# Performance work log

Hardware: AMD Instinct MI355X
Metric: run time of the kernel (lower is better)

The kernel has to match this reference:

```python
import jax, jax.numpy as jnp
import numpy as np

B, T, D, H = 512, 64, 16, 1024  # H must equal T*D (required by the original reshape)


def setup_inputs() -> dict:
    key = jax.random.key(0)
    ks = list(jax.random.split(key, 30))
    def nrm(k, shape, s=0.05):
        return jax.random.normal(k, shape, dtype=jnp.float32) * s
    inp = {}
    inp["values"] = jax.random.normal(ks[0], (B, T, D), dtype=jnp.float32)
    inp["masks"] = (jax.random.uniform(ks[1], (B, T, D)) < 0.8).astype(jnp.float32)
    i = 2
    for pre in ("fw", "bw"):
        for l, din in ((0, D), (1, H)):
            inp[f"{pre}_Wih{l}"] = nrm(ks[i], (4 * H, din)); i += 1
            inp[f"{pre}_Whh{l}"] = nrm(ks[i], (4 * H, H)); i += 1
            inp[f"{pre}_bih{l}"] = nrm(ks[i], (4 * H,)); i += 1
            inp[f"{pre}_bhh{l}"] = nrm(ks[i], (4 * H,)); i += 1
    inp["out_W"] = nrm(ks[i], (D, H)); i += 1
    inp["out_b"] = nrm(ks[i], (D,)); i += 1
    inp["fcb_W"] = nrm(ks[i], (D, 1)); i += 1
    inp["fcb_b"] = nrm(ks[i], (D,)); i += 1
    inp["fce_W"] = nrm(ks[i], (D, 1)); i += 1
    inp["fce_b"] = nrm(ks[i], (D,)); i += 1
    return inp


def _lstm_cell(x, h, c, Wih, Whh, bih, bhh):
    # PyTorch LSTMCell: gate order i, f, g, o
    gates = x @ Wih.T + bih + h @ Whh.T + bhh
    i, f, g, o = jnp.split(gates, 4, axis=-1)
    c2 = jax.nn.sigmoid(f) * c + jax.nn.sigmoid(i) * jnp.tanh(g)
    return jax.nn.sigmoid(o) * jnp.tanh(c2), c2


def _forward(values, masks, fw_Wih0, fw_Whh0, fw_bih0, fw_bhh0, fw_Wih1, fw_Whh1, fw_bih1, fw_bhh1,
             bw_Wih0, bw_Whh0, bw_bih0, bw_bhh0, bw_Wih1, bw_Whh1, bw_bih1, bw_bhh1,
             out_W, out_b, fcb_W, fcb_b, fce_W, fce_b):
    Bc, Tc, Dc = values.shape
    zeros = jnp.zeros((Bc, H), values.dtype)
    bwd_values = jnp.flip(values, 1)
    bwd_masks = jnp.flip(masks, 1)
    # fc_begin/fc_end outputs are dead code in the original (init loop starts at layer 1)
    # Original pre-loop: layers 1..L-1 run once with zero inputs/states.
    hf1, cf1 = _lstm_cell(zeros, zeros, zeros, fw_Wih1, fw_Whh1, fw_bih1, fw_bhh1)
    hb1, cb1 = _lstm_cell(zeros, zeros, zeros, bw_Wih1, bw_Whh1, bw_bih1, bw_bhh1)
    carry0 = (zeros, zeros, hf1, cf1, zeros, zeros, hb1, cb1)

    def step(carry, xs):
        hf0, cf0, hf1, cf1, hb0, cb0, hb1, cb1 = carry
        x_f, m_f, x_b, m_b = xs
        cc_f = (1.0 - m_f) * (hf1 @ out_W.T + out_b) + m_f * x_f
        cc_b = (1.0 - m_b) * (hb1 @ out_W.T + out_b) + m_b * x_b
        hf0, cf0 = _lstm_cell(cc_f, hf0, cf0, fw_Wih0, fw_Whh0, fw_bih0, fw_bhh0)
        hf1, cf1 = _lstm_cell(hf0, hf1, cf1, fw_Wih1, fw_Whh1, fw_bih1, fw_bhh1)
        hb0, cb0 = _lstm_cell(cc_b, hb0, cb0, bw_Wih0, bw_Whh0, bw_bih0, bw_bhh0)
        hb1, cb1 = _lstm_cell(hb0, hb1, cb1, bw_Wih1, bw_Whh1, bw_bih1, bw_bhh1)
        return (hf0, cf0, hf1, cf1, hb0, cb0, hb1, cb1), None

    xs = (jnp.swapaxes(values, 0, 1), jnp.swapaxes(masks, 0, 1),
          jnp.swapaxes(bwd_values, 0, 1), jnp.swapaxes(bwd_masks, 0, 1))
    carry, _ = jax.lax.scan(step, carry0, xs)
    hf1, hb1 = carry[2], carry[6]
    # Original averages fwd with hidden-dim-flipped bwd hidden state
    h = (hf1 + jnp.flip(hb1, 1)) * 0.5
    imputations = h.reshape(Bc, Tc, Dc)
    imputed = imputations * (1.0 - masks) + values * masks
    return h, imputations, imputed


def reference(values, masks, fw_Wih0, fw_Whh0, fw_bih0, fw_bhh0, fw_Wih1, fw_Whh1, fw_bih1, fw_bhh1,
              bw_Wih0, bw_Whh0, bw_bih0, bw_bhh0, bw_Wih1, bw_Whh1, bw_bih1, bw_bhh1,
              out_W, out_b, fcb_W, fcb_b, fce_W, fce_b):
    return _forward(values, masks, fw_Wih0, fw_Whh0, fw_bih0, fw_bhh0, fw_Wih1, fw_Whh1, fw_bih1, fw_bhh1,
                    bw_Wih0, bw_Whh0, bw_bih0, bw_bhh0, bw_Wih1, bw_Whh1, bw_bih1, bw_bhh1,
                    out_W, out_b, fcb_W, fcb_b, fce_W, fce_b)
```

## Files before the change

kernel.cpp:

```cpp
#include <hip/hip_runtime.h>
#include <cstdint>
#include <cstddef>

typedef unsigned short u16;
typedef __attribute__((ext_vector_type(8))) short short8;
typedef __attribute__((ext_vector_type(4))) short short4v;
typedef __attribute__((ext_vector_type(4))) float f32x4;

#define NB 512
#define NT 64
#define ND 16
#define NH 1024

__device__ __forceinline__ u16 f2bf(float x) {
  union { float f; unsigned u; } v; v.f = x;
  unsigned r = v.u + 0x7fffu + ((v.u >> 16) & 1u);
  return (u16)(r >> 16);
}
__device__ __forceinline__ float bf2f(u16 u) {
  union { float f; unsigned u; } v; v.u = ((unsigned)u) << 16;
  return v.f;
}
__device__ __forceinline__ float sigf(float x) { return 1.f / (1.f + __expf(-x)); }

__device__ __forceinline__ int swz(int row, int col) {
  return ((((col >> 3) ^ (row & 7)) << 3) | (col & 7));
}

__device__ __forceinline__ int inv_np(int np) {
  int hb = np >> 6, g = (np >> 4) & 3, hlo = np & 15;
  return g * 1024 + hb * 16 + hlo;
}

__global__ void k_prep_big(const float* s0, const float* s1, const float* s2,
                           const float* s3, const float* s4, const float* s5, u16* dst) {
  for (unsigned q = blockIdx.x * 256 + threadIdx.x; q < (6u << 20); q += gridDim.x * 256) {
    int mat = q >> 20;
    int rem = q & ((1 << 20) - 1);
    int np = rem >> 8;
    int k = (rem & 255) * 4;
    int row = inv_np(np);
    const float* s = mat == 0 ? s0 : mat == 1 ? s1 : mat == 2 ? s2 : mat == 3 ? s3 : mat == 4 ? s4 : s5;
    float4 v = *(const float4*)(s + (size_t)row * NH + k);
    int nb = np >> 4, fr = np & 15, kb = k >> 5, fq = (k >> 3) & 3, e = k & 7;
    u16* d = dst + (size_t)mat * 4194304 + (size_t)((nb * 32 + kb) * 64 + fq * 16 + fr) * 8 + e;
    d[0] = f2bf(v.x); d[1] = f2bf(v.y); d[2] = f2bf(v.z); d[3] = f2bf(v.w);
  }
}

__global__ void k_prep_small(const float* fwih0, const float* bwih0,
                             const float* fbi0, const float* fbh0, const float* fbi1, const float* fbh1,
                             const float* bbi0, const float* bbh0, const float* bbi1, const float* bbh1,
                             const float* outW,
                             u16* wih0p, float* biasb, u16* owbf) {
  int idx = blockIdx.x * 256 + threadIdx.x;
  if (idx < 524288) {
    int dir = idx >> 18;
    int r = idx & 262143;
    int np = r >> 6, d = r & 63;
    int row = inv_np(np);
    const float* s = dir ? bwih0 : fwih0;
    float v = (d < 16) ? s[row * 16 + d] : 0.f;
    int nb = np >> 4, fr = np & 15, kb = d >> 5, fq = (d >> 3) & 3, e = d & 7;
    wih0p[(size_t)dir * 262144 + (size_t)((nb * 2 + kb) * 64 + fq * 16 + fr) * 8 + e] = f2bf(v);
  } else if (idx < 524288 + 16384) {
    int j = idx - 524288;
    int which = j >> 12;
    int np = j & 4095;
    int row = inv_np(np);
    const float* bi = which == 0 ? fbi0 : which == 1 ? fbi1 : which == 2 ? bbi0 : bbi1;
    const float* bh = which == 0 ? fbh0 : which == 1 ? fbh1 : which == 2 ? bbh0 : bbh1;
    biasb[which * 4096 + np] = bi[row] + bh[row];
  } else if (idx < 524288 + 16384 + 16384) {
    int j = idx - 524288 - 16384;
    owbf[j] = f2bf(outW[j]);
  }
}

__global__ void k_init(const float* fbi1, const float* fbh1, const float* bbi1, const float* bbh1,
                       float* c0, float* c1, u16* h0bf, u16* h1bf) {
  int idx = blockIdx.x * 256 + threadIdx.x;
  int dir = idx >> 19;
  int rem = idx & ((1 << 19) - 1);
  int b = rem >> 10, h = rem & 1023;
  const float* bi = dir ? bbi1 : fbi1;
  const float* bh = dir ? bbh1 : fbh1;
  float gi = bi[h] + bh[h];
  float gg = bi[2048 + h] + bh[2048 + h];
  float go = bi[3072 + h] + bh[3072 + h];
  float c = sigf(gi) * tanhf(gg);
  float hv = sigf(go) * tanhf(c);
  size_t o = (size_t)dir * 524288 + rem;
  c1[o] = c;
  h1bf[(size_t)(dir * 2) * 524288 + (size_t)b * NH + swz(b, h)] = f2bf(hv);
  c0[o] = 0.f;
  h0bf[(size_t)(dir * 2) * 524288 + rem] = 0;
}

__global__ __launch_bounds__(256) void k_cc0(const u16* h1f, const u16* h1b,
                                             const float* outW, float* partial) {
  int dir = blockIdx.y;
  int w = threadIdx.x >> 6, lane = threadIdx.x & 63;
  int b = blockIdx.x * 4 + w;
  const u16* hb = dir ? h1b : h1f;
  int key = b & 7;
  short8 ha = *(const short8*)(hb + (size_t)b * NH + ((lane * 2) ^ key) * 8);
  short8 hc = *(const short8*)(hb + (size_t)b * NH + ((lane * 2 + 1) ^ key) * 8);
  float hf[16];
#pragma unroll
  for (int j = 0; j < 8; ++j) { hf[j] = bf2f((u16)ha[j]); hf[8 + j] = bf2f((u16)hc[j]); }
  float sums[16];
#pragma unroll
  for (int d = 0; d < 16; ++d) {
    const float* wr = outW + (size_t)d * NH + lane * 16;
    float s = 0.f;
#pragma unroll
    for (int j = 0; j < 16; ++j) s += hf[j] * wr[j];
#pragma unroll
    for (int off = 32; off; off >>= 1) s += __shfl_xor(s, off);
    sums[d] = s;
  }
  if (lane == 0) {
    float* dst = partial + (size_t)dir * 524288 + (size_t)b * 16;
#pragma unroll
    for (int d = 0; d < 16; ++d) dst[d] = sums[d];
  }
}

struct Frags { short8 a[4]; short8 b[8]; };

__device__ __forceinline__ void domfma(const Frags& F, f32x4 (&acc)[2][4]) {
#pragma unroll
  for (int kk = 0; kk < 2; ++kk)
#pragma unroll
    for (int mi = 0; mi < 2; ++mi)
#pragma unroll
      for (int ni = 0; ni < 4; ++ni)
        acc[mi][ni] = __builtin_amdgcn_mfma_f32_16x16x32_bf16(F.a[mi * 2 + kk], F.b[ni * 2 + kk],
                                                              acc[mi][ni], 0, 0, 0);
}

struct StepCtx {
  u16* h0bf; u16* h1bf;
  const u16* wbig; const u16* wih0p;
  const float* biasb;
  float* c0; float* c1;
  float* partial;
  const float* values; const float* masks; const float* outb;
  const u16* owbf;
};

__device__ __forceinline__ void phase_g0(u16* SM, const StepCtx& a, int dir,
                                         int m_blk, int n_blk, int t, int p) {
  const int m0 = m_blk * 64, n0 = n_blk * 128;
  const int tid = threadIdx.x, w = tid >> 6, lane = tid & 63;
  const int wm = w >> 1, wn = w & 1;
  const int fr = lane & 15, fq = lane >> 4, key = fr & 7;
  const int lane8 = lane * 8;
  const int nbb = n_blk * 8 + wn * 4;
  const u16* h0_in = a.h0bf + (size_t)(dir * 2 + p) * 524288;
  u16* h0_out = a.h0bf + (size_t)(dir * 2 + 1 - p) * 524288;
  const u16* W00 = a.wbig + (size_t)(dir * 3 + 0) * 4194304;
  const u16* Wcc = a.wih0p + (size_t)dir * 262144;
  const float* bias0 = a.biasb + (size_t)dir * 2 * 4096;
  float* cs0 = a.c0 + (size_t)dir * 524288;
  const u16* hA = h0_in + (size_t)m0 * NH;

  int voffA[4];
#pragma unroll
  for (int mi = 0; mi < 2; ++mi)
#pragma unroll
    for (int kk = 0; kk < 2; ++kk)
      voffA[mi * 2 + kk] = (wm * 32 + mi * 16 + fr) * NH + ((fq + kk * 4) ^ key) * 8;

  f32x4 acc[2][4];
#pragma unroll
  for (int i = 0; i < 2; ++i)
#pragma unroll
    for (int j = 0; j < 4; ++j) acc[i][j] = f32x4{0.f, 0.f, 0.f, 0.f};

  Frags f0, fA, fB;
#pragma unroll
  for (int ni = 0; ni < 4; ++ni)
#pragma unroll
    for (int kk = 0; kk < 2; ++kk)
      f0.b[ni * 2 + kk] = *(const short8*)(Wcc + (size_t)((nbb + ni) * 2 + kk) * 512 + lane8);
  auto LD0 = [&](int c, Frags& F) {
    int ci = c - 1;
#pragma unroll
    for (int i = 0; i < 4; ++i) F.a[i] = *(const short8*)(hA + ci * 64 + voffA[i]);
#pragma unroll
    for (int ni = 0; ni < 4; ++ni)
#pragma unroll
      for (int kk = 0; kk < 2; ++kk)
        F.b[ni * 2 + kk] = *(const short8*)(W00 + (size_t)((nbb + ni) * 32 + ci * 2 + kk) * 512 + lane8);
  };
  LD0(1, fA); LD0(2, fB);

  {
    const int rl = tid >> 2, q = tid & 3;
    const int grow = m0 + rl;
    const int d4 = q * 4;
    float4 ps = {0.f, 0.f, 0.f, 0.f};
    const float* pp = a.partial + (size_t)dir * 524288 + (size_t)grow * 16 + d4;
    for (int nb = 0; nb < 64; ++nb) {
      float4 v = *(const float4*)(pp + (size_t)nb * 8192);
      ps.x += v.x; ps.y += v.y; ps.z += v.z; ps.w += v.w;
    }
    int tt = dir ? (NT - 1 - t) : t;
    float4 x = *(const float4*)(a.values + ((size_t)grow * NT + tt) * ND + d4);
    float4 m = *(const float4*)(a.masks + ((size_t)grow * NT + tt) * ND + d4);
    float4 ob = *(const float4*)(a.outb + d4);
    short4v cc;
    cc[0] = (short)f2bf((1.f - m.x) * (ps.x + ob.x) + m.x * x.x);
    cc[1] = (short)f2bf((1.f - m.y) * (ps.y + ob.y) + m.y * x.y);
    cc[2] = (short)f2bf((1.f - m.z) * (ps.z + ob.z) + m.z * x.z);
    cc[3] = (short)f2bf((1.f - m.w) * (ps.w + ob.w) + m.w * x.w);
    int k2 = rl & 7;
    *(short4v*)(SM + rl * 64 + (((d4 >> 3) ^ k2) << 3) + (d4 & 7)) = cc;
    short8 z8 = {0, 0, 0, 0, 0, 0, 0, 0};
    *(short8*)(SM + rl * 64 + (((2 + q) ^ k2) << 3)) = z8;
    if (q < 2) *(short8*)(SM + rl * 64 + (((6 + q) ^ k2) << 3)) = z8;
    asm volatile("s_waitcnt lgkmcnt(0)" ::: "memory");
    __builtin_amdgcn_sched_barrier(0);
  }
  __builtin_amdgcn_s_barrier();

#pragma unroll
  for (int mi = 0; mi < 2; ++mi)
#pragma unroll
    for (int kk = 0; kk < 2; ++kk)
      f0.a[mi * 2 + kk] = *(const short8*)(SM + (wm * 32 + mi * 16 + fr) * 64 + ((fq + kk * 4) ^ key) * 8);
  domfma(f0, acc);
  for (int c = 1; c < 17; c += 2) {
    domfma(fA, acc);
    if (c + 2 < 17) LD0(c + 2, fA);
    domfma(fB, acc);
    if (c + 3 < 17) LD0(c + 3, fB);
  }

  const int hg = ((n0 + wn * 64) >> 2) + fr;
  const float b0 = bias0[n0 + wn * 64 + fr];
  const float b1 = bias0[n0 + wn * 64 + 16 + fr];
  const float b2 = bias0[n0 + wn * 64 + 32 + fr];
  const float b3 = bias0[n0 + wn * 64 + 48 + fr];
#pragma unroll
  for (int mi = 0; mi < 2; ++mi)
#pragma unroll
    for (int r = 0; r < 4; ++r) {
      int row = m0 + wm * 32 + mi * 16 + fq * 4 + r;
      size_t sidx = (size_t)row * NH + hg;
      float iv = acc[mi][0][r] + b0;
      float fv = acc[mi][1][r] + b1;
      float gv = acc[mi][2][r] + b2;
      float ov = acc[mi][3][r] + b3;
      float cp = cs0[sidx];
      float c2 = sigf(fv) * cp + sigf(iv) * tanhf(gv);
      float hvv = sigf(ov) * tanhf(c2);
      cs0[sidx] = c2;
      h0_out[(size_t)row * NH + swz(row, hg)] = f2bf(hvv);
    }
}

__device__ __forceinline__ void phase_g1(u16* SM, const StepCtx& a, int dir,
                                         int m_blk, int n_blk, int t, int p) {
  const int m0 = m_blk * 64, n0 = n_blk * 128;
  const int tid = threadIdx.x, w = tid >> 6, lane = tid & 63;
  const int wm = w >> 1, wn = w & 1;
  const int fr = lane & 15, fq = lane >> 4, key = fr & 7;
  const int lane8 = lane * 8;
  const int nbb = n_blk * 8 + wn * 4;
  const u16* h0_new = a.h0bf + (size_t)(dir * 2 + 1 - p) * 524288;
  const u16* h1_in = a.h1bf + (size_t)(dir * 2 + p) * 524288;
  u16* h1_out = a.h1bf + (size_t)(dir * 2 + 1 - p) * 524288;
  const u16* W10 = a.wbig + (size_t)(dir * 3 + 1) * 4194304;
  const u16* W11 = a.wbig + (size_t)(dir * 3 + 2) * 4194304;
  const float* bias1 = a.biasb + (size_t)(dir * 2 + 1) * 4096;
  float* cs1 = a.c1 + (size_t)dir * 524288;
  const u16* hA0 = h0_new + (size_t)m0 * NH;
  const u16* hA1 = h1_in + (size_t)m0 * NH;

  int voffA[4];
#pragma unroll
  for (int mi = 0; mi < 2; ++mi)
#pragma unroll
    for (int kk = 0; kk < 2; ++kk)
      voffA[mi * 2 + kk] = (wm * 32 + mi * 16 + fr) * NH + ((fq + kk * 4) ^ key) * 8;

  f32x4 acc[2][4];
#pragma unroll
  for (int i = 0; i < 2; ++i)
#pragma unroll
    for (int j = 0; j < 4; ++j) acc[i][j] = f32x4{0.f, 0.f, 0.f, 0.f};

  auto LD1 = [&](int c, Frags& F) {
    const u16* ha = (c < 16) ? hA0 : hA1;
    const u16* wb = (c < 16) ? W10 : W11;
    int ci = (c < 16) ? c : c - 16;
#pragma unroll
    for (int i = 0; i < 4; ++i) F.a[i] = *(const short8*)(ha + ci * 64 + voffA[i]);
#pragma unroll
    for (int ni = 0; ni < 4; ++ni)
#pragma unroll
      for (int kk = 0; kk < 2; ++kk)
        F.b[ni * 2 + kk] = *(const short8*)(wb + (size_t)((nbb + ni) * 32 + ci * 2 + kk) * 512 + lane8);
  };

  Frags fA, fB;
  LD1(0, fA); LD1(1, fB);
  for (int c = 0; c < 32; c += 2) {
    domfma(fA, acc);
    if (c + 2 < 32) LD1(c + 2, fA);
    domfma(fB, acc);
    if (c + 3 < 32) LD1(c + 3, fB);
  }

  const int hb4 = (n0 + wn * 64) >> 2;
  const int hg = hb4 + fr;
  const float b0 = bias1[n0 + wn * 64 + fr];
  const float b1 = bias1[n0 + wn * 64 + 16 + fr];
  const float b2 = bias1[n0 + wn * 64 + 32 + fr];
  const float b3 = bias1[n0 + wn * 64 + 48 + fr];
  float hsv[2][4];
#pragma unroll
  for (int mi = 0; mi < 2; ++mi)
#pragma unroll
    for (int r = 0; r < 4; ++r) {
      int row = m0 + wm * 32 + mi * 16 + fq * 4 + r;
      size_t sidx = (size_t)row * NH + hg;
      float iv = acc[mi][0][r] + b0;
      float fv = acc[mi][1][r] + b1;
      float gv = acc[mi][2][r] + b2;
      float ov = acc[mi][3][r] + b3;
      float cp = cs1[sidx];
      float c2 = sigf(fv) * cp + sigf(iv) * tanhf(gv);
      float hvv = sigf(ov) * tanhf(c2);
      cs1[sidx] = c2;
      h1_out[(size_t)row * NH + swz(row, hg)] = f2bf(hvv);
      hsv[mi][r] = hvv;
    }

  {
    u16* ts = SM + w * 512;
    *(short4v*)(ts + (lane >> 2) * 32 + 16 + (lane & 3) * 4) = short4v{0, 0, 0, 0};
    short8 afr = {0, 0, 0, 0, 0, 0, 0, 0};
    if (fq < 2) afr = *(const short8*)(a.owbf + (size_t)fr * NH + hb4 + fq * 8);
    float* pout = a.partial + ((size_t)(dir * 64 + n_blk * 2 + wn) * 512) * 16;
#pragma unroll
    for (int mi = 0; mi < 2; ++mi) {
#pragma unroll
      for (int r = 0; r < 4; ++r)
        *(ts + (fq * 4 + r) * 32 + fr) = f2bf(hsv[mi][r]);
      asm volatile("s_waitcnt lgkmcnt(0)" ::: "memory");
      __builtin_amdgcn_sched_barrier(0);
      short8 bfr2 = *(const short8*)(ts + fr * 32 + fq * 8);
      f32x4 pz = {0.f, 0.f, 0.f, 0.f};
      pz = __builtin_amdgcn_mfma_f32_16x16x32_bf16(afr, bfr2, pz, 0, 0, 0);
      int row = m0 + wm * 32 + mi * 16 + fr;
      float4 st = {pz[0], pz[1], pz[2], pz[3]};
      *(float4*)(pout + (size_t)row * 16 + fq * 4) = st;
      asm volatile("s_waitcnt lgkmcnt(0)" ::: "memory");
      __builtin_amdgcn_sched_barrier(0);
    }
  }
}

__global__ __launch_bounds__(256) void k_g0(StepCtx a, int t) {
  __shared__ u16 SM[4096];
  phase_g0(SM, a, blockIdx.z, blockIdx.y, blockIdx.x, t, t & 1);
}
__global__ __launch_bounds__(256) void k_g1(StepCtx a, int t) {
  __shared__ u16 SM[4096];
  phase_g1(SM, a, blockIdx.z, blockIdx.y, blockIdx.x, t, t & 1);
}

__global__ void k_final(const u16* hf1, const u16* hb1, const float* values,
                        const float* masks, float* out) {
  int idx = blockIdx.x * 256 + threadIdx.x;
  int b = idx >> 10, j = idx & 1023;
  float hf = bf2f(hf1[(size_t)b * NH + swz(b, j)]);
  int jr = NH - 1 - j;
  float hb = bf2f(hb1[(size_t)b * NH + swz(b, jr)]);
  float hv = 0.5f * (hf + hb);
  float m = masks[idx];
  out[idx] = hv;
  out[524288 + idx] = hv;
  out[1048576 + idx] = hv * (1.f - m) + values[idx] * m;
}

extern "C" void kernel_launch(void* const* d_in, const int* in_sizes, int n_in,
                              void* d_out, int out_size, void* d_ws, size_t ws_size,
                              hipStream_t stream) {
  const float* values  = (const float*)d_in[0];
  const float* masks   = (const float*)d_in[1];
  const float* fw_Wih0 = (const float*)d_in[2];
  const float* fw_Whh0 = (const float*)d_in[3];
  const float* fw_bih0 = (const float*)d_in[4];
  const float* fw_bhh0 = (const float*)d_in[5];
  const float* fw_Wih1 = (const float*)d_in[6];
  const float* fw_Whh1 = (const float*)d_in[7];
  const float* fw_bih1 = (const float*)d_in[8];
  const float* fw_bhh1 = (const float*)d_in[9];
  const float* bw_Wih0 = (const float*)d_in[10];
  const float* bw_Whh0 = (const float*)d_in[11];
  const float* bw_bih0 = (const float*)d_in[12];
  const float* bw_bhh0 = (const float*)d_in[13];
  const float* bw_Wih1 = (const float*)d_in[14];
  const float* bw_Whh1 = (const float*)d_in[15];
  const float* bw_bih1 = (const float*)d_in[16];
  const float* bw_bhh1 = (const float*)d_in[17];
  const float* out_W   = (const float*)d_in[18];
  const float* out_b   = (const float*)d_in[19];

  char* ws = (char*)d_ws;
  u16* wbig    = (u16*)ws;
  u16* wih0p   = (u16*)(ws + 50331648);
  float* biasb = (float*)(ws + 51380224);
  u16* owbf    = (u16*)(ws + 51445760);
  float* c0    = (float*)(ws + 51478528);
  float* c1    = (float*)(ws + 55672832);
  u16* h0bf    = (u16*)(ws + 59867136);
  u16* h1bf    = (u16*)(ws + 64061440);
  float* partial = (float*)(ws + 68255744);
  if (ws_size < 72450048) return;

  k_prep_big<<<4096, 256, 0, stream>>>(fw_Whh0, fw_Wih1, fw_Whh1, bw_Whh0, bw_Wih1, bw_Whh1, wbig);
  k_prep_small<<<2176, 256, 0, stream>>>(fw_Wih0, bw_Wih0, fw_bih0, fw_bhh0, fw_bih1, fw_bhh1,
                                         bw_bih0, bw_bhh0, bw_bih1, bw_bhh1, out_W,
                                         wih0p, biasb, owbf);
  k_init<<<4096, 256, 0, stream>>>(fw_bih1, fw_bhh1, bw_bih1, bw_bhh1, c0, c1, h0bf, h1bf);
  hipMemsetAsync(partial, 0, 4194304, stream);
  k_cc0<<<dim3(128, 2), 256, 0, stream>>>(h1bf, h1bf + (size_t)2 * 524288, out_W, partial);

  StepCtx sc;
  sc.h0bf = h0bf; sc.h1bf = h1bf;
  sc.wbig = wbig; sc.wih0p = wih0p;
  sc.biasb = biasb; sc.c0 = c0; sc.c1 = c1;
  sc.partial = partial;
  sc.values = values; sc.masks = masks; sc.outb = out_b;
  sc.owbf = owbf;

  for (int t = 0; t < NT; ++t) {
    k_g0<<<dim3(32, 8, 2), 256, 0, stream>>>(sc, t);
    k_g1<<<dim3(32, 8, 2), 256, 0, stream>>>(sc, t);
  }

  k_final<<<2048, 256, 0, stream>>>(h1bf, h1bf + (size_t)2 * 524288, values, masks, (float*)d_out);
}
```

Measured before the change: 3.781 ms.

## Stage hidden-state A tiles through LDS with async global_load_lds multi-buffering

The recurrent GEMM kernels now copy the activation (A) tiles into a 4-deep LDS ring using global_load_lds, wait on them with explicit vmcnt counters and block barriers, and keep a triple-buffered register pipeline for the weight (B) fragments. This replaces direct global loads of A fragments per wave, which duplicated reads across waves, with shared staging and deeper prefetch, at the cost of more LDS per block and more barriers. Launch bounds now request two blocks per CU. The weight-prep kernel is also rewritten so each thread writes one coalesced 16-byte packed chunk, and the partial-sum reduction uses two accumulators.

```diff
diff --git a/kernel.cpp b/kernel.cpp
--- a/kernel.cpp
+++ b/kernel.cpp
@@ -12,6 +12,8 @@
 #define ND 16
 #define NH 1024
 
+#define WAITV(N) asm volatile("s_waitcnt vmcnt(" #N ")" ::: "memory")
+
 __device__ __forceinline__ u16 f2bf(float x) {
   union { float f; unsigned u; } v; v.f = x;
   unsigned r = v.u + 0x7fffu + ((v.u >> 16) & 1u);
@@ -23,6 +25,11 @@
 }
 __device__ __forceinline__ float sigf(float x) { return 1.f / (1.f + __expf(-x)); }
 
+__device__ __forceinline__ void glds16(const void* g, void* l) {
+  __builtin_amdgcn_global_load_lds((const __attribute__((address_space(1))) void*)g,
+                                   (__attribute__((address_space(3))) void*)l, 16, 0, 0);
+}
+
 __device__ __forceinline__ int swz(int row, int col) {
   return ((((col >> 3) ^ (row & 7)) << 3) | (col & 7));
 }
@@ -34,18 +41,22 @@
 
 __global__ void k_prep_big(const float* s0, const float* s1, const float* s2,
                            const float* s3, const float* s4, const float* s5, u16* dst) {
-  for (unsigned q = blockIdx.x * 256 + threadIdx.x; q < (6u << 20); q += gridDim.x * 256) {
-    int mat = q >> 20;
-    int rem = q & ((1 << 20) - 1);
-    int np = rem >> 8;
-    int k = (rem & 255) * 4;
-    int row = inv_np(np);
-    const float* s = mat == 0 ? s0 : mat == 1 ? s1 : mat == 2 ? s2 : mat == 3 ? s3 : mat == 4 ? s4 : s5;
-    float4 v = *(const float4*)(s + (size_t)row * NH + k);
-    int nb = np >> 4, fr = np & 15, kb = k >> 5, fq = (k >> 3) & 3, e = k & 7;
-    u16* d = dst + (size_t)mat * 4194304 + (size_t)((nb * 32 + kb) * 64 + fq * 16 + fr) * 8 + e;
-    d[0] = f2bf(v.x); d[1] = f2bf(v.y); d[2] = f2bf(v.z); d[3] = f2bf(v.w);
-  }
+  unsigned q = blockIdx.x * 256 + threadIdx.x;
+  int mat = q >> 19;
+  int r = q & ((1 << 19) - 1);
+  int nb = r >> 11, kb = (r >> 6) & 31, l = r & 63;
+  int fr = l & 15, fq = l >> 4;
+  int np = nb * 16 + fr;
+  int row = inv_np(np);
+  int k0 = kb * 32 + fq * 8;
+  const float* s = mat == 0 ? s0 : mat == 1 ? s1 : mat == 2 ? s2 : mat == 3 ? s3 : mat == 4 ? s4 : s5;
+  const float* sr = s + (size_t)row * NH + k0;
+  float4 v0 = *(const float4*)sr;
+  float4 v1 = *(const float4*)(sr + 4);
+  short8 o;
+  o[0] = (short)f2bf(v0.x); o[1] = (short)f2bf(v0.y); o[2] = (short)f2bf(v0.z); o[3] = (short)f2bf(v0.w);
+  o[4] = (short)f2bf(v1.x); o[5] = (short)f2bf(v1.y); o[6] = (short)f2bf(v1.z); o[7] = (short)f2bf(v1.w);
+  *(short8*)(dst + (size_t)q * 8) = o;
 }
 
 __global__ void k_prep_small(const float* fwih0, const float* bwih0,
@@ -127,18 +138,7 @@
   }
 }
 
-struct Frags { short8 a[4]; short8 b[8]; };
-
-__device__ __forceinline__ void domfma(const Frags& F, f32x4 (&acc)[2][4]) {
-#pragma unroll
-  for (int kk = 0; kk < 2; ++kk)
-#pragma unroll
-    for (int mi = 0; mi < 2; ++mi)
-#pragma unroll
-      for (int ni = 0; ni < 4; ++ni)
-        acc[mi][ni] = __builtin_amdgcn_mfma_f32_16x16x32_bf16(F.a[mi * 2 + kk], F.b[ni * 2 + kk],
-                                                              acc[mi][ni], 0, 0, 0);
-}
+struct BF { short8 b[8]; };
 
 struct StepCtx {
   u16* h0bf; u16* h1bf;
@@ -150,10 +150,13 @@
   const u16* owbf;
 };
 
-__device__ __forceinline__ void phase_g0(u16* SM, const StepCtx& a, int dir,
-                                         int m_blk, int n_blk, int t, int p) {
+__global__ __launch_bounds__(256, 2) void k_g0(StepCtx a, int t) {
+  __shared__ u16 SM[5 * 4096];
+  const int dir = blockIdx.z, m_blk = blockIdx.y, n_blk = blockIdx.x;
+  const int p = t & 1;
   const int m0 = m_blk * 64, n0 = n_blk * 128;
   const int tid = threadIdx.x, w = tid >> 6, lane = tid & 63;
+  const int srow = lane >> 3, scol = (lane & 7) * 8;
   const int wm = w >> 1, wn = w & 1;
   const int fr = lane & 15, fq = lane >> 4, key = fr & 7;
   const int lane8 = lane * 8;
@@ -164,14 +167,13 @@
   const u16* Wcc = a.wih0p + (size_t)dir * 262144;
   const float* bias0 = a.biasb + (size_t)dir * 2 * 4096;
   float* cs0 = a.c0 + (size_t)dir * 524288;
-  const u16* hA = h0_in + (size_t)m0 * NH;
-
-  int voffA[4];
+
+  int aoff[4];
 #pragma unroll
   for (int mi = 0; mi < 2; ++mi)
 #pragma unroll
     for (int kk = 0; kk < 2; ++kk)
-      voffA[mi * 2 + kk] = (wm * 32 + mi * 16 + fr) * NH + ((fq + kk * 4) ^ key) * 8;
+      aoff[mi * 2 + kk] = (wm * 32 + mi * 16 + fr) * 64 + ((fq + kk * 4) ^ key) * 8;
 
   f32x4 acc[2][4];
 #pragma unroll
@@ -179,34 +181,66 @@
 #pragma unroll
     for (int j = 0; j < 4; ++j) acc[i][j] = f32x4{0.f, 0.f, 0.f, 0.f};
 
-  Frags f0, fA, fB;
-#pragma unroll
-  for (int ni = 0; ni < 4; ++ni)
-#pragma unroll
-    for (int kk = 0; kk < 2; ++kk)
-      f0.b[ni * 2 + kk] = *(const short8*)(Wcc + (size_t)((nbb + ni) * 2 + kk) * 512 + lane8);
-  auto LD0 = [&](int c, Frags& F) {
+  auto stageA = [&](int c) {
+    u16* lb = SM + (c & 3) * 4096;
+    const u16* pa = h0_in + (size_t)(c - 1) * 64;
+    glds16(pa + (size_t)(m0 + w * 16 + srow) * NH + scol, lb + (w * 16) * 64);
+    glds16(pa + (size_t)(m0 + w * 16 + 8 + srow) * NH + scol, lb + (w * 16 + 8) * 64);
+  };
+  auto LDB = [&](int c, BF& F) {
     int ci = c - 1;
-#pragma unroll
-    for (int i = 0; i < 4; ++i) F.a[i] = *(const short8*)(hA + ci * 64 + voffA[i]);
 #pragma unroll
     for (int ni = 0; ni < 4; ++ni)
 #pragma unroll
       for (int kk = 0; kk < 2; ++kk)
         F.b[ni * 2 + kk] = *(const short8*)(W00 + (size_t)((nbb + ni) * 32 + ci * 2 + kk) * 512 + lane8);
   };
-  LD0(1, fA); LD0(2, fB);
+  auto domfma = [&](const short8 (&af)[4], const BF& B) {
+#pragma unroll
+    for (int kk = 0; kk < 2; ++kk)
+#pragma unroll
+      for (int mi = 0; mi < 2; ++mi)
+#pragma unroll
+        for (int ni = 0; ni < 4; ++ni)
+          acc[mi][ni] = __builtin_amdgcn_mfma_f32_16x16x32_bf16(af[mi * 2 + kk], B.b[ni * 2 + kk],
+                                                                acc[mi][ni], 0, 0, 0);
+  };
+  auto DO = [&](int x, BF& B, int st, int lb) {
+    __builtin_amdgcn_s_barrier();
+    __builtin_amdgcn_sched_barrier(0);
+    if (st >= 0) stageA(st);
+    short8 af[4];
+    const u16* base = SM + (x & 3) * 4096;
+#pragma unroll
+    for (int i = 0; i < 4; ++i) af[i] = *(const short8*)(base + aoff[i]);
+    domfma(af, B);
+    if (lb >= 0) LDB(lb, B);
+  };
+
+  BF Ba, Bb, Bc;
+#pragma unroll
+  for (int ni = 0; ni < 4; ++ni)
+#pragma unroll
+    for (int kk = 0; kk < 2; ++kk)
+      Ba.b[ni * 2 + kk] = *(const short8*)(Wcc + (size_t)((nbb + ni) * 2 + kk) * 512 + lane8);
+  stageA(1); stageA(2); stageA(3);
+  LDB(1, Bb); LDB(2, Bc);
 
   {
+    u16* SM4 = SM + 4 * 4096;
     const int rl = tid >> 2, q = tid & 3;
     const int grow = m0 + rl;
     const int d4 = q * 4;
-    float4 ps = {0.f, 0.f, 0.f, 0.f};
+    float4 ps0 = {0.f, 0.f, 0.f, 0.f}, ps1 = {0.f, 0.f, 0.f, 0.f};
     const float* pp = a.partial + (size_t)dir * 524288 + (size_t)grow * 16 + d4;
-    for (int nb = 0; nb < 64; ++nb) {
-      float4 v = *(const float4*)(pp + (size_t)nb * 8192);
-      ps.x += v.x; ps.y += v.y; ps.z += v.z; ps.w += v.w;
+#pragma unroll 4
+    for (int nb = 0; nb < 64; nb += 2) {
+      float4 v0 = *(const float4*)(pp + (size_t)nb * 8192);
+      float4 v1 = *(const float4*)(pp + (size_t)(nb + 1) * 8192);
+      ps0.x += v0.x; ps0.y += v0.y; ps0.z += v0.z; ps0.w += v0.w;
+      ps1.x += v1.x; ps1.y += v1.y; ps1.z += v1.z; ps1.w += v1.w;
     }
+    float4 ps = {ps0.x + ps1.x, ps0.y + ps1.y, ps0.z + ps1.z, ps0.w + ps1.w};
     int tt = dir ? (NT - 1 - t) : t;
     float4 x = *(const float4*)(a.values + ((size_t)grow * NT + tt) * ND + d4);
     float4 m = *(const float4*)(a.masks + ((size_t)grow * NT + tt) * ND + d4);
@@ -217,27 +251,33 @@
     cc[2] = (short)f2bf((1.f - m.z) * (ps.z + ob.z) + m.z * x.z);
     cc[3] = (short)f2bf((1.f - m.w) * (ps.w + ob.w) + m.w * x.w);
     int k2 = rl & 7;
-    *(short4v*)(SM + rl * 64 + (((d4 >> 3) ^ k2) << 3) + (d4 & 7)) = cc;
+    *(short4v*)(SM4 + rl * 64 + (((d4 >> 3) ^ k2) << 3) + (d4 & 7)) = cc;
     short8 z8 = {0, 0, 0, 0, 0, 0, 0, 0};
-    *(short8*)(SM + rl * 64 + (((2 + q) ^ k2) << 3)) = z8;
-    if (q < 2) *(short8*)(SM + rl * 64 + (((6 + q) ^ k2) << 3)) = z8;
+    *(short8*)(SM4 + rl * 64 + (((2 + q) ^ k2) << 3)) = z8;
+    if (q < 2) *(short8*)(SM4 + rl * 64 + (((6 + q) ^ k2) << 3)) = z8;
     asm volatile("s_waitcnt lgkmcnt(0)" ::: "memory");
     __builtin_amdgcn_sched_barrier(0);
   }
+
   __builtin_amdgcn_s_barrier();
-
-#pragma unroll
-  for (int mi = 0; mi < 2; ++mi)
-#pragma unroll
-    for (int kk = 0; kk < 2; ++kk)
-      f0.a[mi * 2 + kk] = *(const short8*)(SM + (wm * 32 + mi * 16 + fr) * 64 + ((fq + kk * 4) ^ key) * 8);
-  domfma(f0, acc);
-  for (int c = 1; c < 17; c += 2) {
-    domfma(fA, acc);
-    if (c + 2 < 17) LD0(c + 2, fA);
-    domfma(fB, acc);
-    if (c + 3 < 17) LD0(c + 3, fB);
-  }
+  __builtin_amdgcn_sched_barrier(0);
+  {
+    short8 af[4];
+    const u16* SM4 = SM + 4 * 4096;
+#pragma unroll
+    for (int i = 0; i < 4; ++i) af[i] = *(const short8*)(SM4 + aoff[i]);
+    domfma(af, Ba);
+    LDB(3, Ba);
+  }
+  for (int c = 1; c < 13; c += 3) {
+    WAITV(28); DO(c, Bb, c + 3, c + 3);
+    WAITV(28); DO(c + 1, Bc, c + 4, c + 4);
+    WAITV(28); DO(c + 2, Ba, c + 5, c + 5);
+  }
+  WAITV(28); DO(13, Bb, 16, 16);
+  WAITV(28); DO(14, Bc, -1, -1);
+  WAITV(18); DO(15, Ba, -1, -1);
+  WAITV(8);  DO(16, Bb, -1, -1);
 
   const int hg = ((n0 + wn * 64) >> 2) + fr;
   const float b0 = bias0[n0 + wn * 64 + fr];
@@ -262,10 +302,13 @@
     }
 }
 
-__device__ __forceinline__ void phase_g1(u16* SM, const StepCtx& a, int dir,
-                                         int m_blk, int n_blk, int t, int p) {
+__global__ __launch_bounds__(256, 2) void k_g1(StepCtx a, int t) {
+  __shared__ u16 SM[4 * 4096];
+  const int dir = blockIdx.z, m_blk = blockIdx.y, n_blk = blockIdx.x;
+  const int p = t & 1;
   const int m0 = m_blk * 64, n0 = n_blk * 128;
   const int tid = threadIdx.x, w = tid >> 6, lane = tid & 63;
+  const int srow = lane >> 3, scol = (lane & 7) * 8;
   const int wm = w >> 1, wn = w & 1;
   const int fr = lane & 15, fq = lane >> 4, key = fr & 7;
   const int lane8 = lane * 8;
@@ -277,15 +320,13 @@
   const u16* W11 = a.wbig + (size_t)(dir * 3 + 2) * 4194304;
   const float* bias1 = a.biasb + (size_t)(dir * 2 + 1) * 4096;
   float* cs1 = a.c1 + (size_t)dir * 524288;
-  const u16* hA0 = h0_new + (size_t)m0 * NH;
-  const u16* hA1 = h1_in + (size_t)m0 * NH;
-
-  int voffA[4];
+
+  int aoff[4];
 #pragma unroll
   for (int mi = 0; mi < 2; ++mi)
 #pragma unroll
     for (int kk = 0; kk < 2; ++kk)
-      voffA[mi * 2 + kk] = (wm * 32 + mi * 16 + fr) * NH + ((fq + kk * 4) ^ key) * 8;
+      aoff[mi * 2 + kk] = (wm * 32 + mi * 16 + fr) * 64 + ((fq + kk * 4) ^ key) * 8;
 
   f32x4 acc[2][4];
 #pragma unroll
@@ -293,27 +334,57 @@
 #pragma unroll
     for (int j = 0; j < 4; ++j) acc[i][j] = f32x4{0.f, 0.f, 0.f, 0.f};
 
-  auto LD1 = [&](int c, Frags& F) {
-    const u16* ha = (c < 16) ? hA0 : hA1;
+  auto stageA = [&](int c) {
+    u16* lb = SM + (c & 3) * 4096;
+    const u16* pa = (c < 16) ? (h0_new + (size_t)c * 64) : (h1_in + (size_t)(c - 16) * 64);
+    glds16(pa + (size_t)(m0 + w * 16 + srow) * NH + scol, lb + (w * 16) * 64);
+    glds16(pa + (size_t)(m0 + w * 16 + 8 + srow) * NH + scol, lb + (w * 16 + 8) * 64);
+  };
+  auto LDB = [&](int c, BF& F) {
     const u16* wb = (c < 16) ? W10 : W11;
     int ci = (c < 16) ? c : c - 16;
 #pragma unroll
-    for (int i = 0; i < 4; ++i) F.a[i] = *(const short8*)(ha + ci * 64 + voffA[i]);
-#pragma unroll
     for (int ni = 0; ni < 4; ++ni)
 #pragma unroll
       for (int kk = 0; kk < 2; ++kk)
         F.b[ni * 2 + kk] = *(const short8*)(wb + (size_t)((nbb + ni) * 32 + ci * 2 + kk) * 512 + lane8);
   };
-
-  Frags fA, fB;
-  LD1(0, fA); LD1(1, fB);
-  for (int c = 0; c < 32; c += 2) {
-    domfma(fA, acc);
-    if (c + 2 < 32) LD1(c + 2, fA);
-    domfma(fB, acc);
-    if (c + 3 < 32) LD1(c + 3, fB);
-  }
+  auto domfma = [&](const short8 (&af)[4], const BF& B) {
+#pragma unroll
+    for (int kk = 0; kk < 2; ++kk)
+#pragma unroll
+      for (int mi = 0; mi < 2; ++mi)
+#pragma unroll
+        for (int ni = 0; ni < 4; ++ni)
+          acc[mi][ni] = __builtin_amdgcn_mfma_f32_16x16x32_bf16(af[mi * 2 + kk], B.b[ni * 2 + kk],
+                                                                acc[mi][ni], 0, 0, 0);
+  };
+  auto DO = [&](int x, BF& B, int st, int lb) {
+    __builtin_amdgcn_s_barrier();
+    __builtin_amdgcn_sched_barrier(0);
+    if (st >= 0) stageA(st);
+    short8 af[4];
+    const u16* base = SM + (x & 3) * 4096;
+#pragma unroll
+    for (int i = 0; i < 4; ++i) af[i] = *(const short8*)(base + aoff[i]);
+    domfma(af, B);
+    if (lb >= 0) LDB(lb, B);
+  };
+
+  BF Ba, Bb, Bc;
+  stageA(0); stageA(1); stageA(2);
+  LDB(0, Ba); LDB(1, Bb); LDB(2, Bc);
+
+  for (int c = 0; c < 27; c += 3) {
+    WAITV(28); DO(c, Ba, c + 3, c + 3);
+    WAITV(28); DO(c + 1, Bb, c + 4, c + 4);
+    WAITV(28); DO(c + 2, Bc, c + 5, c + 5);
+  }
+  WAITV(28); DO(27, Ba, 30, 30);
+  WAITV(28); DO(28, Bb, 31, 31);
+  WAITV(28); DO(29, Bc, -1, -1);
+  WAITV(18); DO(30, Ba, -1, -1);
+  WAITV(8);  DO(31, Bb, -1, -1);
 
   const int hb4 = (n0 + wn * 64) >> 2;
   const int hg = hb4 + fr;
@@ -363,15 +434,6 @@
       __builtin_amdgcn_sched_barrier(0);
     }
   }
-}
-
-__global__ __launch_bounds__(256) void k_g0(StepCtx a, int t) {
-  __shared__ u16 SM[4096];
-  phase_g0(SM, a, blockIdx.z, blockIdx.y, blockIdx.x, t, t & 1);
-}
-__global__ __launch_bounds__(256) void k_g1(StepCtx a, int t) {
-  __shared__ u16 SM[4096];
-  phase_g1(SM, a, blockIdx.z, blockIdx.y, blockIdx.x, t, t & 1);
 }
 
 __global__ void k_final(const u16* hf1, const u16* hb1, const float* values,
@@ -424,7 +486,7 @@
   float* partial = (float*)(ws + 68255744);
   if (ws_size < 72450048) return;
 
-  k_prep_big<<<4096, 256, 0, stream>>>(fw_Whh0, fw_Wih1, fw_Whh1, bw_Whh0, bw_Wih1, bw_Whh1, wbig);
+  k_prep_big<<<12288, 256, 0, stream>>>(fw_Whh0, fw_Wih1, fw_Whh1, bw_Whh0, bw_Wih1, bw_Whh1, wbig);
   k_prep_small<<<2176, 256, 0, stream>>>(fw_Wih0, bw_Wih0, fw_bih0, fw_bhh0, fw_bih1, fw_bhh1,
                                          bw_bih0, bw_bhh0, bw_bih1, bw_bhh1, out_W,
                                          wih0p, biasb, owbf);
```

After: 5.812 ms. 53.7% more time.

## Stage LSTM weight tiles into LDS via async global_load_lds triple buffering

Applied to the files above, without the earlier changes.

Weight matrices are repacked into a row-major swizzled layout, and the per-step gate GEMMs now stream each 128x64 weight tile into shared memory with global_load_lds. The stream uses a three-stage ring buffer with vmcnt waits and barriers. Each weight fragment is loaded once per block and shared by the warps, instead of every warp pulling its own fragments from global memory into registers. The goal is to cut redundant global weight traffic and register pressure (the launch bounds now target 2 blocks per CU), at the cost of extra block barriers and more shared memory. The partial-sum reduction loop also gains a second accumulator for more memory-level parallelism.

```diff
diff --git a/kernel.cpp b/kernel.cpp
--- a/kernel.cpp
+++ b/kernel.cpp
@@ -12,6 +12,9 @@
 #define ND 16
 #define NH 1024
 
+#define WAITV(N) asm volatile("s_waitcnt vmcnt(" #N ")" ::: "memory")
+#define BARR __builtin_amdgcn_s_barrier(); __builtin_amdgcn_sched_barrier(0)
+
 __device__ __forceinline__ u16 f2bf(float x) {
   union { float f; unsigned u; } v; v.f = x;
   unsigned r = v.u + 0x7fffu + ((v.u >> 16) & 1u);
@@ -22,6 +25,11 @@
   return v.f;
 }
 __device__ __forceinline__ float sigf(float x) { return 1.f / (1.f + __expf(-x)); }
+
+__device__ __forceinline__ void glds16(const void* g, void* l) {
+  __builtin_amdgcn_global_load_lds((const __attribute__((address_space(1))) void*)g,
+                                   (__attribute__((address_space(3))) void*)l, 16, 0, 0);
+}
 
 __device__ __forceinline__ int swz(int row, int col) {
   return ((((col >> 3) ^ (row & 7)) << 3) | (col & 7));
@@ -42,8 +50,7 @@
     int row = inv_np(np);
     const float* s = mat == 0 ? s0 : mat == 1 ? s1 : mat == 2 ? s2 : mat == 3 ? s3 : mat == 4 ? s4 : s5;
     float4 v = *(const float4*)(s + (size_t)row * NH + k);
-    int nb = np >> 4, fr = np & 15, kb = k >> 5, fq = (k >> 3) & 3, e = k & 7;
-    u16* d = dst + (size_t)mat * 4194304 + (size_t)((nb * 32 + kb) * 64 + fq * 16 + fr) * 8 + e;
+    u16* d = dst + (size_t)mat * 4194304 + (size_t)np * NH + swz(np, k);
     d[0] = f2bf(v.x); d[1] = f2bf(v.y); d[2] = f2bf(v.z); d[3] = f2bf(v.w);
   }
 }
@@ -61,8 +68,7 @@
     int row = inv_np(np);
     const float* s = dir ? bwih0 : fwih0;
     float v = (d < 16) ? s[row * 16 + d] : 0.f;
-    int nb = np >> 4, fr = np & 15, kb = d >> 5, fq = (d >> 3) & 3, e = d & 7;
-    wih0p[(size_t)dir * 262144 + (size_t)((nb * 2 + kb) * 64 + fq * 16 + fr) * 8 + e] = f2bf(v);
+    wih0p[(size_t)dir * 262144 + (size_t)np * 64 + swz(np, d)] = f2bf(v);
   } else if (idx < 524288 + 16384) {
     int j = idx - 524288;
     int which = j >> 12;
@@ -127,18 +133,7 @@
   }
 }
 
-struct Frags { short8 a[4]; short8 b[8]; };
-
-__device__ __forceinline__ void domfma(const Frags& F, f32x4 (&acc)[2][4]) {
-#pragma unroll
-  for (int kk = 0; kk < 2; ++kk)
-#pragma unroll
-    for (int mi = 0; mi < 2; ++mi)
-#pragma unroll
-      for (int ni = 0; ni < 4; ++ni)
-        acc[mi][ni] = __builtin_amdgcn_mfma_f32_16x16x32_bf16(F.a[mi * 2 + kk], F.b[ni * 2 + kk],
-                                                              acc[mi][ni], 0, 0, 0);
-}
+struct AF { short8 a[4]; };
 
 struct StepCtx {
   u16* h0bf; u16* h1bf;
@@ -150,14 +145,15 @@
   const u16* owbf;
 };
 
-__device__ __forceinline__ void phase_g0(u16* SM, const StepCtx& a, int dir,
-                                         int m_blk, int n_blk, int t, int p) {
+__global__ __launch_bounds__(256, 2) void k_g0(StepCtx a, int t) {
+  __shared__ u16 SM[3 * 8192 + 4096];
+  const int dir = blockIdx.z, m_blk = blockIdx.y, n_blk = blockIdx.x;
+  const int p = t & 1;
   const int m0 = m_blk * 64, n0 = n_blk * 128;
   const int tid = threadIdx.x, w = tid >> 6, lane = tid & 63;
+  const int srow = lane >> 3, scol = (lane & 7) * 8;
   const int wm = w >> 1, wn = w & 1;
   const int fr = lane & 15, fq = lane >> 4, key = fr & 7;
-  const int lane8 = lane * 8;
-  const int nbb = n_blk * 8 + wn * 4;
   const u16* h0_in = a.h0bf + (size_t)(dir * 2 + p) * 524288;
   u16* h0_out = a.h0bf + (size_t)(dir * 2 + 1 - p) * 524288;
   const u16* W00 = a.wbig + (size_t)(dir * 3 + 0) * 4194304;
@@ -165,13 +161,21 @@
   const float* bias0 = a.biasb + (size_t)dir * 2 * 4096;
   float* cs0 = a.c0 + (size_t)dir * 524288;
   const u16* hA = h0_in + (size_t)m0 * NH;
-
-  int voffA[4];
+  u16* SMX = SM + 3 * 8192;
+
+  int aoffg[4], aoffs[4], boff[8];
 #pragma unroll
   for (int mi = 0; mi < 2; ++mi)
 #pragma unroll
+    for (int kk = 0; kk < 2; ++kk) {
+      aoffg[mi * 2 + kk] = (wm * 32 + mi * 16 + fr) * NH + ((fq + kk * 4) ^ key) * 8;
+      aoffs[mi * 2 + kk] = (wm * 32 + mi * 16 + fr) * 64 + ((fq + kk * 4) ^ key) * 8;
+    }
+#pragma unroll
+  for (int ni = 0; ni < 4; ++ni)
+#pragma unroll
     for (int kk = 0; kk < 2; ++kk)
-      voffA[mi * 2 + kk] = (wm * 32 + mi * 16 + fr) * NH + ((fq + kk * 4) ^ key) * 8;
+      boff[ni * 2 + kk] = (wn * 64 + ni * 16 + fr) * 64 + ((fq + kk * 4) ^ key) * 8;
 
   f32x4 acc[2][4];
 #pragma unroll
@@ -179,34 +183,52 @@
 #pragma unroll
     for (int j = 0; j < 4; ++j) acc[i][j] = f32x4{0.f, 0.f, 0.f, 0.f};
 
-  Frags f0, fA, fB;
-#pragma unroll
-  for (int ni = 0; ni < 4; ++ni)
-#pragma unroll
-    for (int kk = 0; kk < 2; ++kk)
-      f0.b[ni * 2 + kk] = *(const short8*)(Wcc + (size_t)((nbb + ni) * 2 + kk) * 512 + lane8);
-  auto LD0 = [&](int c, Frags& F) {
-    int ci = c - 1;
-#pragma unroll
-    for (int i = 0; i < 4; ++i) F.a[i] = *(const short8*)(hA + ci * 64 + voffA[i]);
+  auto stageB = [&](int c, int buf) {
+    u16* lb = SM + buf * 8192;
+    const u16* pw = W00 + (size_t)(c - 1) * 64;
+#pragma unroll
+    for (int k = 0; k < 4; ++k)
+      glds16(pw + (size_t)(n0 + w * 32 + k * 8 + srow) * NH + scol, lb + (w * 32 + k * 8) * 64);
+  };
+  auto ldA = [&](int c, AF& F) {
+    const u16* pa = hA + (size_t)(c - 1) * 64;
+#pragma unroll
+    for (int i = 0; i < 4; ++i) F.a[i] = *(const short8*)(pa + aoffg[i]);
+  };
+  auto comp = [&](int buf, const AF& F) {
+    const u16* base = SM + buf * 8192;
 #pragma unroll
     for (int ni = 0; ni < 4; ++ni)
 #pragma unroll
-      for (int kk = 0; kk < 2; ++kk)
-        F.b[ni * 2 + kk] = *(const short8*)(W00 + (size_t)((nbb + ni) * 32 + ci * 2 + kk) * 512 + lane8);
-  };
-  LD0(1, fA); LD0(2, fB);
+      for (int kk = 0; kk < 2; ++kk) {
+        short8 bfrag = *(const short8*)(base + boff[ni * 2 + kk]);
+#pragma unroll
+        for (int mi = 0; mi < 2; ++mi)
+          acc[mi][ni] = __builtin_amdgcn_mfma_f32_16x16x32_bf16(F.a[mi * 2 + kk], bfrag, acc[mi][ni], 0, 0, 0);
+      }
+  };
+
+  AF Aa, Ab, Ac;
+#pragma unroll
+  for (int k = 0; k < 4; ++k)
+    glds16(Wcc + (size_t)(n0 + w * 32 + k * 8 + srow) * 64 + scol, SM + (w * 32 + k * 8) * 64);
+  stageB(1, 1); ldA(1, Ab);
+  __builtin_amdgcn_sched_barrier(0);
 
   {
     const int rl = tid >> 2, q = tid & 3;
     const int grow = m0 + rl;
     const int d4 = q * 4;
-    float4 ps = {0.f, 0.f, 0.f, 0.f};
+    float4 ps0 = {0.f, 0.f, 0.f, 0.f}, ps1 = {0.f, 0.f, 0.f, 0.f};
     const float* pp = a.partial + (size_t)dir * 524288 + (size_t)grow * 16 + d4;
-    for (int nb = 0; nb < 64; ++nb) {
-      float4 v = *(const float4*)(pp + (size_t)nb * 8192);
-      ps.x += v.x; ps.y += v.y; ps.z += v.z; ps.w += v.w;
+#pragma unroll 4
+    for (int nb = 0; nb < 64; nb += 2) {
+      float4 v0 = *(const float4*)(pp + (size_t)nb * 8192);
+      float4 v1 = *(const float4*)(pp + (size_t)(nb + 1) * 8192);
+      ps0.x += v0.x; ps0.y += v0.y; ps0.z += v0.z; ps0.w += v0.w;
+      ps1.x += v1.x; ps1.y += v1.y; ps1.z += v1.z; ps1.w += v1.w;
     }
+    float4 ps = {ps0.x + ps1.x, ps0.y + ps1.y, ps0.z + ps1.z, ps0.w + ps1.w};
     int tt = dir ? (NT - 1 - t) : t;
     float4 x = *(const float4*)(a.values + ((size_t)grow * NT + tt) * ND + d4);
     float4 m = *(const float4*)(a.masks + ((size_t)grow * NT + tt) * ND + d4);
@@ -217,27 +239,31 @@
     cc[2] = (short)f2bf((1.f - m.z) * (ps.z + ob.z) + m.z * x.z);
     cc[3] = (short)f2bf((1.f - m.w) * (ps.w + ob.w) + m.w * x.w);
     int k2 = rl & 7;
-    *(short4v*)(SM + rl * 64 + (((d4 >> 3) ^ k2) << 3) + (d4 & 7)) = cc;
+    *(short4v*)(SMX + rl * 64 + (((d4 >> 3) ^ k2) << 3) + (d4 & 7)) = cc;
     short8 z8 = {0, 0, 0, 0, 0, 0, 0, 0};
-    *(short8*)(SM + rl * 64 + (((2 + q) ^ k2) << 3)) = z8;
-    if (q < 2) *(short8*)(SM + rl * 64 + (((6 + q) ^ k2) << 3)) = z8;
+    *(short8*)(SMX + rl * 64 + (((2 + q) ^ k2) << 3)) = z8;
+    if (q < 2) *(short8*)(SMX + rl * 64 + (((6 + q) ^ k2) << 3)) = z8;
     asm volatile("s_waitcnt lgkmcnt(0)" ::: "memory");
     __builtin_amdgcn_sched_barrier(0);
   }
-  __builtin_amdgcn_s_barrier();
-
-#pragma unroll
-  for (int mi = 0; mi < 2; ++mi)
-#pragma unroll
-    for (int kk = 0; kk < 2; ++kk)
-      f0.a[mi * 2 + kk] = *(const short8*)(SM + (wm * 32 + mi * 16 + fr) * 64 + ((fq + kk * 4) ^ key) * 8);
-  domfma(f0, acc);
-  for (int c = 1; c < 17; c += 2) {
-    domfma(fA, acc);
-    if (c + 2 < 17) LD0(c + 2, fA);
-    domfma(fB, acc);
-    if (c + 3 < 17) LD0(c + 3, fB);
-  }
+
+  WAITV(8); BARR;
+  stageB(2, 2); ldA(2, Ac);
+  {
+    AF F0;
+#pragma unroll
+    for (int i = 0; i < 4; ++i) F0.a[i] = *(const short8*)(SMX + aoffs[i]);
+    comp(0, F0);
+  }
+  WAITV(8); BARR; stageB(3, 0); ldA(3, Aa); comp(1, Ab);
+  for (int c = 2; c < 14; c += 3) {
+    WAITV(8); BARR; stageB(c + 2, 1); ldA(c + 2, Ab); comp(2, Ac);
+    WAITV(8); BARR; stageB(c + 3, 2); ldA(c + 3, Ac); comp(0, Aa);
+    WAITV(8); BARR; stageB(c + 4, 0); ldA(c + 4, Aa); comp(1, Ab);
+  }
+  WAITV(8); BARR; stageB(16, 1); ldA(16, Ab); comp(2, Ac);
+  WAITV(8); BARR; comp(0, Aa);
+  WAITV(0); BARR; comp(1, Ab);
 
   const int hg = ((n0 + wn * 64) >> 2) + fr;
   const float b0 = bias0[n0 + wn * 64 + fr];
@@ -262,14 +288,15 @@
     }
 }
 
-__device__ __forceinline__ void phase_g1(u16* SM, const StepCtx& a, int dir,
-                                         int m_blk, int n_blk, int t, int p) {
+__global__ __launch_bounds__(256, 2) void k_g1(StepCtx a, int t) {
+  __shared__ u16 SM[3 * 8192];
+  const int dir = blockIdx.z, m_blk = blockIdx.y, n_blk = blockIdx.x;
+  const int p = t & 1;
   const int m0 = m_blk * 64, n0 = n_blk * 128;
   const int tid = threadIdx.x, w = tid >> 6, lane = tid & 63;
+  const int srow = lane >> 3, scol = (lane & 7) * 8;
   const int wm = w >> 1, wn = w & 1;
   const int fr = lane & 15, fq = lane >> 4, key = fr & 7;
-  const int lane8 = lane * 8;
-  const int nbb = n_blk * 8 + wn * 4;
   const u16* h0_new = a.h0bf + (size_t)(dir * 2 + 1 - p) * 524288;
   const u16* h1_in = a.h1bf + (size_t)(dir * 2 + p) * 524288;
   u16* h1_out = a.h1bf + (size_t)(dir * 2 + 1 - p) * 524288;
@@ -280,12 +307,17 @@
   const u16* hA0 = h0_new + (size_t)m0 * NH;
   const u16* hA1 = h1_in + (size_t)m0 * NH;
 
-  int voffA[4];
+  int aoffg[4], boff[8];
 #pragma unroll
   for (int mi = 0; mi < 2; ++mi)
 #pragma unroll
     for (int kk = 0; kk < 2; ++kk)
-      voffA[mi * 2 + kk] = (wm * 32 + mi * 16 + fr) * NH + ((fq + kk * 4) ^ key) * 8;
+      aoffg[mi * 2 + kk] = (wm * 32 + mi * 16 + fr) * NH + ((fq + kk * 4) ^ key) * 8;
+#pragma unroll
+  for (int ni = 0; ni < 4; ++ni)
+#pragma unroll
+    for (int kk = 0; kk < 2; ++kk)
+      boff[ni * 2 + kk] = (wn * 64 + ni * 16 + fr) * 64 + ((fq + kk * 4) ^ key) * 8;
 
   f32x4 acc[2][4];
 #pragma unroll
@@ -293,27 +325,43 @@
 #pragma unroll
     for (int j = 0; j < 4; ++j) acc[i][j] = f32x4{0.f, 0.f, 0.f, 0.f};
 
-  auto LD1 = [&](int c, Frags& F) {
-    const u16* ha = (c < 16) ? hA0 : hA1;
-    const u16* wb = (c < 16) ? W10 : W11;
-    int ci = (c < 16) ? c : c - 16;
-#pragma unroll
-    for (int i = 0; i < 4; ++i) F.a[i] = *(const short8*)(ha + ci * 64 + voffA[i]);
+  auto stageB = [&](int c, int buf) {
+    u16* lb = SM + buf * 8192;
+    const u16* pw = (c < 16) ? (W10 + (size_t)c * 64) : (W11 + (size_t)(c - 16) * 64);
+#pragma unroll
+    for (int k = 0; k < 4; ++k)
+      glds16(pw + (size_t)(n0 + w * 32 + k * 8 + srow) * NH + scol, lb + (w * 32 + k * 8) * 64);
+  };
+  auto ldA = [&](int c, AF& F) {
+    const u16* pa = (c < 16) ? (hA0 + (size_t)c * 64) : (hA1 + (size_t)(c - 16) * 64);
+#pragma unroll
+    for (int i = 0; i < 4; ++i) F.a[i] = *(const short8*)(pa + aoffg[i]);
+  };
+  auto comp = [&](int buf, const AF& F) {
+    const u16* base = SM + buf * 8192;
 #pragma unroll
     for (int ni = 0; ni < 4; ++ni)
 #pragma unroll
-      for (int kk = 0; kk < 2; ++kk)
-        F.b[ni * 2 + kk] = *(const short8*)(wb + (size_t)((nbb + ni) * 32 + ci * 2 + kk) * 512 + lane8);
-  };
-
-  Frags fA, fB;
-  LD1(0, fA); LD1(1, fB);
-  for (int c = 0; c < 32; c += 2) {
-    domfma(fA, acc);
-    if (c + 2 < 32) LD1(c + 2, fA);
-    domfma(fB, acc);
-    if (c + 3 < 32) LD1(c + 3, fB);
-  }
+      for (int kk = 0; kk < 2; ++kk) {
+        short8 bfrag = *(const short8*)(base + boff[ni * 2 + kk]);
+#pragma unroll
+        for (int mi = 0; mi < 2; ++mi)
+          acc[mi][ni] = __builtin_amdgcn_mfma_f32_16x16x32_bf16(F.a[mi * 2 + kk], bfrag, acc[mi][ni], 0, 0, 0);
+      }
+  };
+
+  AF Aa, Ab, Ac;
+  stageB(0, 0); ldA(0, Aa);
+  stageB(1, 1); ldA(1, Ab);
+  __builtin_amdgcn_sched_barrier(0);
+
+  for (int c = 0; c < 30; c += 3) {
+    WAITV(8); BARR; stageB(c + 2, 2); ldA(c + 2, Ac); comp(0, Aa);
+    WAITV(8); BARR; stageB(c + 3, 0); ldA(c + 3, Aa); comp(1, Ab);
+    WAITV(8); BARR; stageB(c + 4, 1); ldA(c + 4, Ab); comp(2, Ac);
+  }
+  WAITV(8); BARR; comp(0, Aa);
+  WAITV(0); BARR; comp(1, Ab);
 
   const int hb4 = (n0 + wn * 64) >> 2;
   const int hg = hb4 + fr;
@@ -363,15 +411,6 @@
       __builtin_amdgcn_sched_barrier(0);
     }
   }
-}
-
-__global__ __launch_bounds__(256) void k_g0(StepCtx a, int t) {
-  __shared__ u16 SM[4096];
-  phase_g0(SM, a, blockIdx.z, blockIdx.y, blockIdx.x, t, t & 1);
-}
-__global__ __launch_bounds__(256) void k_g1(StepCtx a, int t) {
-  __shared__ u16 SM[4096];
-  phase_g1(SM, a, blockIdx.z, blockIdx.y, blockIdx.x, t, t & 1);
 }
 
 __global__ void k_final(const u16* hf1, const u16* hb1, const float* values,
```

After: 3.268 ms. 13.6% less time.
